# Kernel optimization log

Measured on AMD Instinct MI355X. Metric: run time of the kernel, lower is better.

Reference implementation:

```python
import jax, jax.numpy as jnp
import numpy as np

B, H, D = 8, 1024, 4
K_COUP = 1.0
DT = 1.0


def setup_inputs() -> dict:
    key = jax.random.key(0)
    k1, k2, k3, k4, k5 = jax.random.split(key, 5)
    return {
        "theta_prev": jax.random.normal(k1, (B, H, D), dtype=jnp.float32),
        "gamma": jax.random.normal(k2, (B, H), dtype=jnp.float32),
        "A": jax.random.normal(k3, (B, H, H), dtype=jnp.float32),
        "omega": jax.random.normal(k4, (H, D), dtype=jnp.float32) * 0.1,
        "kappa": jnp.ones((H, D), dtype=jnp.float32),
        "alpha": jax.random.normal(k5, (H, H), dtype=jnp.float32) * 0.1,
    }


def reference(theta_prev, gamma, A, omega, kappa, alpha):
    # theta_prev: [B,H,D], gamma: [B,H], A: [B,H,H]
    Bn, Hn, Dn = theta_prev.shape
    # symmetrize + relu lateral coupling matrix
    A_lat = jax.nn.relu(0.5 * (A + jnp.swapaxes(A, 1, 2)))  # [B,H,H]
    # pairwise phase differences: theta_j - theta_i - alpha -> [B,H,H,D]
    phase_diff = (theta_prev[:, None, :, :] - theta_prev[:, :, None, :]
                  - alpha[None, :, :, None])
    # weighted sum over j axis
    coupling = (K_COUP / Hn) * jnp.sum(A_lat[..., None] * jnp.sin(phase_diff), axis=2)  # [B,H,D]
    theta_dot = omega[None] + coupling + kappa[None] * (gamma[..., None] - theta_prev)
    return theta_prev + DT * theta_dot
```

## Files before the change

### kernel.cpp

```cpp
#include <hip/hip_runtime.h>
#include <math.h>

#define BB 8
#define HH 1024
#define DD 4
#define TI 16
#define JC 256
#define NJC (HH / JC)


__global__ __launch_bounds__(256) void kuramoto_partial(
    const float* __restrict__ theta, const float* __restrict__ A,
    const float* __restrict__ alpha, float* __restrict__ ws)
{
    const int blk = blockIdx.x;
    const int jc  = blk & (NJC - 1);
    const int it  = (blk >> 2) & 63;
    const int b   = blk >> 8;
    const int i0  = it * TI;
    const int j0  = jc * JC;
    const int t   = threadIdx.x;
    const int ti  = t >> 4;
    const int tj  = t & 15;

    __shared__ float4 sThJ[JC];
    __shared__ float  sAT[JC][TI + 1];

    const float* Ab = A + (size_t)b * HH * HH;

    sThJ[t] = ((const float4*)theta)[(size_t)b * HH + j0 + t];

    {
        const int r = t >> 2;
        const int c = (t & 3) * 4;
        #pragma unroll
        for (int rr = 0; rr < JC; rr += 64) {
            const int row = rr + r;
            const float4 v = *(const float4*)&Ab[(size_t)(j0 + row) * HH + i0 + c];
            sAT[row][c + 0] = v.x;
            sAT[row][c + 1] = v.y;
            sAT[row][c + 2] = v.z;
            sAT[row][c + 3] = v.w;
        }
    }
    __syncthreads();

    const float4 thi   = ((const float4*)theta)[(size_t)b * HH + i0 + ti];
    const float* Arow  = Ab    + (size_t)(i0 + ti) * HH + j0;
    const float* alrow = alpha + (size_t)(i0 + ti) * HH + j0;

    float a0 = 0.f, a1 = 0.f, a2 = 0.f, a3 = 0.f;
    #pragma unroll
    for (int s = 0; s < JC / 16; ++s) {
        const int jj = tj + 16 * s;
        const float ad = Arow[jj];
        const float al = alrow[jj];
        const float at = sAT[jj][ti];
        const float alat = fmaxf(0.5f * (ad + at), 0.0f);
        const float4 thj = sThJ[jj];
        a0 += alat * __sinf(thj.x - thi.x - al);
        a1 += alat * __sinf(thj.y - thi.y - al);
        a2 += alat * __sinf(thj.z - thi.z - al);
        a3 += alat * __sinf(thj.w - thi.w - al);
    }

    #pragma unroll
    for (int off = 8; off >= 1; off >>= 1) {
        a0 += __shfl_down(a0, off, 16);
        a1 += __shfl_down(a1, off, 16);
        a2 += __shfl_down(a2, off, 16);
        a3 += __shfl_down(a3, off, 16);
    }

    if (tj == 0) {
        float4 r; r.x = a0; r.y = a1; r.z = a2; r.w = a3;
        ((float4*)ws)[((size_t)jc * BB + b) * HH + i0 + ti] = r;
    }
}

__global__ __launch_bounds__(256) void kuramoto_final(
    const float* __restrict__ theta, const float* __restrict__ gamma,
    const float* __restrict__ omega, const float* __restrict__ kappa,
    const float* __restrict__ ws, float* __restrict__ out)
{
    const int idx = blockIdx.x * 256 + threadIdx.x;
    const int i   = idx & (HH - 1);
    const float4* w4 = (const float4*)ws;

    float4 p = w4[idx];
    #pragma unroll
    for (int jc = 1; jc < NJC; ++jc) {
        const float4 q = w4[(size_t)jc * BB * HH + idx];
        p.x += q.x; p.y += q.y; p.z += q.z; p.w += q.w;
    }

    const float4 th = ((const float4*)theta)[idx];
    const float4 om = ((const float4*)omega)[i];
    const float4 kp = ((const float4*)kappa)[i];
    const float  g  = gamma[idx];
    const float  inv = 1.0f / HH;

    float4 o;
    o.x = th.x + om.x + p.x * inv + kp.x * (g - th.x);
    o.y = th.y + om.y + p.y * inv + kp.y * (g - th.y);
    o.z = th.z + om.z + p.z * inv + kp.z * (g - th.z);
    o.w = th.w + om.w + p.w * inv + kp.w * (g - th.w);
    ((float4*)out)[idx] = o;
}

extern "C" void kernel_launch(void* const* d_in, const int* in_sizes, int n_in,
                              void* d_out, int out_size, void* d_ws, size_t ws_size,
                              hipStream_t stream) {
    const float* theta = (const float*)d_in[0];
    const float* gamma = (const float*)d_in[1];
    const float* A     = (const float*)d_in[2];
    const float* omega = (const float*)d_in[3];
    const float* kappa = (const float*)d_in[4];
    const float* alpha = (const float*)d_in[5];
    float* out = (float*)d_out;
    float* ws  = (float*)d_ws;

    hipLaunchKernelGGL(kuramoto_partial, dim3(BB * (HH / TI) * NJC), dim3(256), 0, stream,
                       theta, A, alpha, ws);
    hipLaunchKernelGGL(kuramoto_final, dim3(BB * HH / 256), dim3(256), 0, stream,
                       theta, gamma, omega, kappa, ws, out);
}
```

Measured before the change: 103.4 us.

## Vectorize A/alpha row loads, split j into more chunks, SoA theta in LDS

Each thread now reads four consecutive A and alpha row elements with one float4 load instead of scalar strided loads. The j dimension is split into 8 chunks of 128 instead of 4 chunks of 256, which doubles the grid, and a launch-bounds occupancy hint is added. The j-side theta values are stored in LDS as four scalar arrays instead of float4. The aim is wider, more coalesced global loads and more parallelism. The cost is more partial sums for the final reduction and possible LDS bank conflicts on the transposed tile reads.

```diff
diff --git a/kernel.cpp b/kernel.cpp
--- a/kernel.cpp
+++ b/kernel.cpp
@@ -5,30 +5,33 @@
 #define HH 1024
 #define DD 4
 #define TI 16
-#define JC 256
-#define NJC (HH / JC)
+#define NJC 8
+#define JC (HH / NJC)
 
 
-__global__ __launch_bounds__(256) void kuramoto_partial(
+__global__ __launch_bounds__(256, 8) void kuramoto_partial(
     const float* __restrict__ theta, const float* __restrict__ A,
     const float* __restrict__ alpha, float* __restrict__ ws)
 {
     const int blk = blockIdx.x;
     const int jc  = blk & (NJC - 1);
-    const int it  = (blk >> 2) & 63;
-    const int b   = blk >> 8;
+    const int it  = (blk >> 3) & 63;
+    const int b   = blk >> 9;
     const int i0  = it * TI;
     const int j0  = jc * JC;
     const int t   = threadIdx.x;
     const int ti  = t >> 4;
     const int tj  = t & 15;
 
-    __shared__ float4 sThJ[JC];
-    __shared__ float  sAT[JC][TI + 1];
+    __shared__ float sTh0[JC], sTh1[JC], sTh2[JC], sTh3[JC];
+    __shared__ float sAT[JC][TI + 1];
 
     const float* Ab = A + (size_t)b * HH * HH;
 
-    sThJ[t] = ((const float4*)theta)[(size_t)b * HH + j0 + t];
+    if (t < JC) {
+        const float4 v = ((const float4*)theta)[(size_t)b * HH + j0 + t];
+        sTh0[t] = v.x; sTh1[t] = v.y; sTh2[t] = v.z; sTh3[t] = v.w;
+    }
 
     {
         const int r = t >> 2;
@@ -45,23 +48,29 @@
     }
     __syncthreads();
 
-    const float4 thi   = ((const float4*)theta)[(size_t)b * HH + i0 + ti];
-    const float* Arow  = Ab    + (size_t)(i0 + ti) * HH + j0;
-    const float* alrow = alpha + (size_t)(i0 + ti) * HH + j0;
+    const float4 thi = ((const float4*)theta)[(size_t)b * HH + i0 + ti];
+    const float4* Arow4  = (const float4*)(Ab    + (size_t)(i0 + ti) * HH + j0);
+    const float4* alrow4 = (const float4*)(alpha + (size_t)(i0 + ti) * HH + j0);
 
     float a0 = 0.f, a1 = 0.f, a2 = 0.f, a3 = 0.f;
+
     #pragma unroll
-    for (int s = 0; s < JC / 16; ++s) {
-        const int jj = tj + 16 * s;
-        const float ad = Arow[jj];
-        const float al = alrow[jj];
-        const float at = sAT[jj][ti];
-        const float alat = fmaxf(0.5f * (ad + at), 0.0f);
-        const float4 thj = sThJ[jj];
-        a0 += alat * __sinf(thj.x - thi.x - al);
-        a1 += alat * __sinf(thj.y - thi.y - al);
-        a2 += alat * __sinf(thj.z - thi.z - al);
-        a3 += alat * __sinf(thj.w - thi.w - al);
+    for (int s = 0; s < JC / 64; ++s) {
+        const int q = tj + 16 * s;
+        const float4 ad = Arow4[q];
+        const float4 al = alrow4[q];
+        const int j = 4 * q;
+        #pragma unroll
+        for (int k = 0; k < 4; ++k) {
+            const float adk = (&ad.x)[k];
+            const float alk = (&al.x)[k];
+            const float at  = sAT[j + k][ti];
+            const float alat = fmaxf(0.5f * (adk + at), 0.0f);
+            a0 += alat * __sinf(sTh0[j + k] - thi.x - alk);
+            a1 += alat * __sinf(sTh1[j + k] - thi.y - alk);
+            a2 += alat * __sinf(sTh2[j + k] - thi.z - alk);
+            a3 += alat * __sinf(sTh3[j + k] - thi.w - alk);
+        }
     }
 
     #pragma unroll
```

After: 93.18 us. -9.9%, faster.
